# Performance work log

Measured on AMD Instinct MI355X. Metric: run time of the kernel, lower is better.

The kernel has to match this reference:

```python
import jax, jax.numpy as jnp
import numpy as np

DIM = 768
NUM_HEADS = 12


def setup_inputs() -> dict:
    key = jax.random.key(0)
    k1, k2, k3 = jax.random.split(key, 3)
    x = jax.random.normal(k1, (8, 32, 32, DIM), dtype=jnp.float32)
    # xavier_uniform-style init for kernels
    lim_qkv = float(np.sqrt(6.0 / (DIM + 3 * DIM)))
    lim_o = float(np.sqrt(6.0 / (DIM + DIM)))
    w_qkv = jax.random.uniform(k2, (DIM, 3 * DIM), jnp.float32, -lim_qkv, lim_qkv)
    w_o = jax.random.uniform(k3, (DIM, DIM), jnp.float32, -lim_o, lim_o)
    return {"x": x, "w_qkv": w_qkv, "w_o": w_o}


def reference(x, w_qkv, w_o):
    bs, h, w, c = x.shape
    n = h * w
    nh = NUM_HEADS
    hd = c // nh
    xt = x.reshape(bs, n, c)
    qkv = xt @ w_qkv                                   # [bs, n, 3c]
    qkv = qkv.reshape(bs, n, 3, nh, hd)
    qkv = jnp.transpose(qkv, (2, 0, 3, 1, 4))          # [3, bs, nh, n, hd]
    q, k, v = qkv[0], qkv[1], qkv[2]
    scale = hd ** -0.5
    attn = jnp.einsum('bhqd,bhkd->bhqk', q, k) * scale  # [bs, nh, n, n]
    attn = jax.nn.softmax(attn, axis=-1)
    out = jnp.einsum('bhqk,bhkd->bhqd', attn, v)       # [bs, nh, n, hd]
    out = out.swapaxes(1, 2).reshape(bs, n, c)
    out = out @ w_o
    side = int(n ** 0.5)
    return out.reshape(bs, side, side, -1)
```

## Files before the change

kernel.cpp:

```cpp
#include <hip/hip_runtime.h>
#include <hip/hip_bf16.h>
#include <stdint.h>
#include <math.h>

#define SEQ   1024
#define NHEAD 12
#define HD    64
#define CDIM  768
#define MTOK  8192
#define NQKV  2304
#define NPAIR 96

#define QSCALE 0.18033688011112042f

typedef uint16_t u16;
typedef __attribute__((ext_vector_type(8)))  __bf16 bf16x8;
typedef __attribute__((ext_vector_type(4)))  float  f32x4;
typedef __attribute__((ext_vector_type(16))) float  f32x16;

__device__ __forceinline__ u16 f32_to_bf16(float f) {
  union { float f; uint32_t u; } cv; cv.f = f;
  uint32_t u = cv.u;
  return (u16)((u + 0x7FFFu + ((u >> 16) & 1u)) >> 16);
}

__device__ __forceinline__ uint32_t cvt_pk_bf16(float lo, float hi) {
  uint32_t r;
  asm("v_cvt_pk_bf16_f32 %0, %1, %2" : "=v"(r) : "v"(lo), "v"(hi));
  return r;
}

__device__ __forceinline__ void pl32_swap(uint32_t& a, uint32_t& b) {
  asm("v_permlane32_swap_b32 %0, %1" : "+v"(a), "+v"(b));
}

__device__ __forceinline__ float vexp2(float x) {
  float r; asm("v_exp_f32 %0, %1" : "=v"(r) : "v"(x)); return r;
}
__device__ __forceinline__ float vmax3(float a, float b, float c) {
  float d; asm("v_max3_f32 %0, %1, %2, %3" : "=v"(d) : "v"(a), "v"(b), "v"(c)); return d;
}
__device__ __forceinline__ float vrcp(float x) {
  float r; asm("v_rcp_f32 %0, %1" : "=v"(r) : "v"(x)); return r;
}

__device__ __forceinline__ void load_lds16(const u16* g, u16* l) {
  __builtin_amdgcn_global_load_lds(
      (const __attribute__((address_space(1))) uint32_t*)g,
      (__attribute__((address_space(3))) uint32_t*)l, 16, 0, 0);
}

__device__ __forceinline__ bf16x8 ldsw(const u16* base, int r, int cb) {
  int byte = (r << 7) + cb;
  byte ^= ((r & 7) << 4);
  return *(const bf16x8*)((const char*)base + byte);
}

template<int NB>
__device__ __forceinline__ void stage_swz(const u16* __restrict__ g, u16* l, int tid) {
  #pragma unroll
  for (int i = 0; i < NB / 4096; ++i) {
    int F = i * 4096 + tid * 16;
    int S = F ^ (((F >> 7) & 7) << 4);
    load_lds16(g + (S >> 1), l + (F >> 1));
  }
}

__device__ __forceinline__ void stage_vt(const u16* __restrict__ vtb, u16* l, int kc, int tid) {
  #pragma unroll
  for (int i = 0; i < 2; ++i) {
    int F = i * 4096 + tid * 16;
    int S = F ^ (((F >> 7) & 7) << 4);
    int r = S >> 7;
    int cb = S & 127;
    load_lds16(vtb + ((size_t)r << 10) + (kc << 6) + (cb >> 1), l + (F >> 1));
  }
}

#define CVT_BLOCKS 3072
#define TQKV_BLOCKS 432
__global__ __launch_bounds__(256) void prep_kernel(const float* __restrict__ x,
                                                   u16* __restrict__ xb,
                                                   const float* __restrict__ wqkv,
                                                   u16* __restrict__ wqkvT,
                                                   const float* __restrict__ wo,
                                                   u16* __restrict__ woT) {
  __shared__ u16 t[64][66];
  int bid = blockIdx.x;
  int tid = threadIdx.x;

  if (bid < CVT_BLOCKS) {
    int i = bid * 256 + tid;
    const float4* p = (const float4*)x + (size_t)i * 2;
    float4 a = p[0], b = p[1];
    uint4 o;
    o.x = cvt_pk_bf16(a.x, a.y);
    o.y = cvt_pk_bf16(a.z, a.w);
    o.z = cvt_pk_bf16(b.x, b.y);
    o.w = cvt_pk_bf16(b.z, b.w);
    ((uint4*)xb)[i] = o;
    return;
  }

  const float* in;
  u16* outp;
  int N, bid2;
  if (bid < CVT_BLOCKS + TQKV_BLOCKS) {
    bid2 = bid - CVT_BLOCKS; in = wqkv; outp = wqkvT; N = NQKV;
  } else {
    bid2 = bid - CVT_BLOCKS - TQKV_BLOCKS; in = wo; outp = woT; N = CDIM;
  }
  const int K = CDIM, nbk = CDIM >> 6;
  int bk = bid2 % nbk, bn = bid2 / nbk;
  int k0 = bk << 6, n0 = bn << 6;
  #pragma unroll
  for (int i = 0; i < 16; ++i) {
    int idx = i * 256 + tid;
    int kr = idx >> 6, nc = idx & 63;
    t[kr][nc] = f32_to_bf16(in[(size_t)(k0 + kr) * N + n0 + nc]);
  }
  __syncthreads();
  #pragma unroll
  for (int i = 0; i < 16; ++i) {
    int idx = i * 256 + tid;
    int nr = idx >> 6, kc = idx & 63;
    outp[(size_t)(n0 + nr) * K + k0 + kc] = t[kc][nr];
  }
}

template<int EPI>
__global__ __launch_bounds__(256) void gemm_bt(const u16* __restrict__ A,
                                               const u16* __restrict__ Bt,
                                               float* __restrict__ Cf,
                                               u16* __restrict__ qb,
                                               u16* __restrict__ kb,
                                               u16* __restrict__ vb,
                                               int M, int N, int K) {
  __shared__ u16 SH[4][8192];

  int bid = blockIdx.x;
  int xcd = bid & 7, ii = bid >> 3;
  int tn = ii >> 3;
  int tm = (xcd << 3) + (ii & 7);
  int mBase = tm << 7, nBase = tn << 7;
  int tid = threadIdx.x;
  int lane = tid & 63, wid = tid >> 6;
  int wr = (wid >> 1) << 6, wc = (wid & 1) << 6;
  int lr = lane & 15, lk = lane >> 4;

  const int nk = K >> 6;

  auto STAGE = [&](int kt, int b) {
    #pragma unroll
    for (int i2 = 0; i2 < 4; ++i2) {
      int F = i2 * 4096 + tid * 16;
      int row = F >> 7;
      int cb  = (F & 127) ^ ((row & 7) << 4);
      load_lds16(A + (size_t)(mBase + row) * K + kt * 64 + (cb >> 1), &SH[b][F >> 1]);
    }
    #pragma unroll
    for (int i2 = 0; i2 < 4; ++i2) {
      int F = i2 * 4096 + tid * 16;
      int row = F >> 7;
      int cb  = (F & 127) ^ ((row & 7) << 4);
      load_lds16(Bt + (size_t)(nBase + row) * K + kt * 64 + (cb >> 1), &SH[2 + b][F >> 1]);
    }
  };

  f32x4 acc[4][4] = {};

  STAGE(0, 0);
  for (int kt = 0; kt < nk; ++kt) {
    const int cur = kt & 1;
    if (kt + 1 < nk) {
      STAGE(kt + 1, cur ^ 1);
      asm volatile("s_waitcnt vmcnt(8)" ::: "memory");
    } else {
      asm volatile("s_waitcnt vmcnt(0)" ::: "memory");
    }
    __builtin_amdgcn_s_barrier();
    asm volatile("" ::: "memory");

    #pragma unroll
    for (int kk = 0; kk < 2; ++kk) {
      bf16x8 af[4], bfr[4];
      #pragma unroll
      for (int i2 = 0; i2 < 4; ++i2)
        af[i2]  = ldsw(SH[cur], wr + i2 * 16 + lr, kk * 64 + lk * 16);
      #pragma unroll
      for (int i2 = 0; i2 < 4; ++i2)
        bfr[i2] = ldsw(SH[2 + cur], wc + i2 * 16 + lr, kk * 64 + lk * 16);
      #pragma unroll
      for (int mi = 0; mi < 4; ++mi)
        #pragma unroll
        for (int ni = 0; ni < 4; ++ni)
          acc[mi][ni] = __builtin_amdgcn_mfma_f32_16x16x32_bf16(af[mi], bfr[ni], acc[mi][ni], 0, 0, 0);
    }

    __builtin_amdgcn_s_barrier();
    asm volatile("" ::: "memory");
  }

  if (EPI == 0) {
    int c0 = nBase + wc;
    int s  = c0 / CDIM;
    int rem0 = c0 - s * CDIM, hh = rem0 >> 6;
    u16* ereg = &SH[0][0] + wid * 4096;

    #pragma unroll
    for (int mi = 0; mi < 4; ++mi)
      #pragma unroll
      for (int ni = 0; ni < 4; ++ni)
        #pragma unroll
        for (int j = 0; j < 4; ++j) {
          float val = acc[mi][ni][j];
          if (s == 0) val *= QSCALE;
          int mloc = mi * 16 + lk * 4 + j;
          int cloc = ni * 16 + lr;
          int rrow = (s == 2) ? cloc : mloc;
          int ccol = (s == 2) ? mloc : cloc;
          int byte = (rrow << 7) + (((ccol << 1)) ^ ((rrow & 7) << 4));
          *(u16*)((char*)ereg + byte) = f32_to_bf16(val);
        }

    u16* dst;
    if (s == 2) {
      int m0 = mBase + wr;
      int bb = m0 >> 10, nn0 = m0 & 1023;
      dst = vb + (((size_t)(bb * NHEAD + hh)) << 16) + ((size_t)lane << 10) + nn0;
    } else {
      int mrow = mBase + wr + lane;
      int bb = mrow >> 10, nn = mrow & 1023;
      u16* buf = (s == 0) ? qb : kb;
      dst = buf + (((size_t)(bb * NHEAD + hh)) << 16) + nn * 64;
    }
    #pragma unroll
    for (int ic = 0; ic < 8; ++ic) {
      int rc = (ic + (lane >> 3)) & 7;
      int byte = (lane << 7) + ((rc << 4) ^ ((lane & 7) << 4));
      bf16x8 vv = *(const bf16x8*)((const char*)ereg + byte);
      *(bf16x8*)(dst + rc * 8) = vv;
    }
  } else {
    char* ereg = (char*)(&SH[0][0]) + wid * 16384;
    #pragma unroll
    for (int mi = 0; mi < 4; ++mi)
      #pragma unroll
      for (int ni = 0; ni < 4; ++ni)
        #pragma unroll
        for (int j = 0; j < 4; ++j) {
          int rrow = mi * 16 + lk * 4 + j;
          int byte = (rrow << 8) + (((ni * 16 + lr) << 2) ^ ((rrow & 7) << 4));
          *(float*)(ereg + byte) = acc[mi][ni][j];
        }
    int mrow = mBase + wr + lane;
    float* dst = Cf + (size_t)mrow * N + (nBase + wc);
    #pragma unroll
    for (int ic = 0; ic < 16; ++ic) {
      int rc = (ic + ((lane >> 3) << 1)) & 15;
      int byte = (lane << 8) + ((rc << 4) ^ ((lane & 7) << 4));
      f32x4 vv = *(const f32x4*)(ereg + byte);
      *(f32x4*)(dst + rc * 4) = vv;
    }
  }
}

__global__ __launch_bounds__(256, 3) void attn_kernel(const u16* __restrict__ q,
                                                      const u16* __restrict__ k,
                                                      const u16* __restrict__ v,
                                                      u16* __restrict__ out) {
  __shared__ u16 Ks[2][4096];
  __shared__ u16 Vs[3][4096];

  int bid = blockIdx.x;
  int wgid = (bid & 7) * 96 + (bid >> 3);
  int pair = wgid >> 3;
  int qt   = wgid & 7;
  int b = pair / NHEAD, hh = pair - b * NHEAD;
  const u16* Kg  = k + ((size_t)pair << 16);
  const u16* Vtb = v + ((size_t)pair << 16);
  int tid = threadIdx.x, lane = tid & 63, wid = tid >> 6;
  int ql = lane & 31, hi = lane >> 5;

  const u16* Qrow = q + ((size_t)pair << 16) + (size_t)((qt << 7) + (wid << 5) + ql) * 64;
  bf16x8 qf[4];
  #pragma unroll
  for (int t = 0; t < 4; ++t)
    qf[t] = *(const bf16x8*)(Qrow + t * 16 + hi * 8);

  float m_ = -1e30f, l_ = 0.f;
  f32x16 acc0 = {}, acc1 = {};
  f32x16 pA0, pA1, pB0, pB1;

  auto SMPV = [&](f32x16& s0, f32x16& s1, const u16* vbase) {
    float a0 = vmax3(s0[0],  s0[1],  s0[2]);
    float a1 = vmax3(s0[3],  s0[4],  s0[5]);
    float a2 = vmax3(s0[6],  s0[7],  s0[8]);
    float a3 = vmax3(s0[9],  s0[10], s0[11]);
    float a4 = vmax3(s0[12], s0[13], s0[14]);
    float a5 = vmax3(s0[15], s1[0],  s1[1]);
    float a6 = vmax3(s1[2],  s1[3],  s1[4]);
    float a7 = vmax3(s1[5],  s1[6],  s1[7]);
    float a8 = vmax3(s1[8],  s1[9],  s1[10]);
    float a9 = vmax3(s1[11], s1[12], s1[13]);
    float aA = fmaxf(s1[14], s1[15]);
    float b0 = vmax3(a0, a1, a2);
    float b1 = vmax3(a3, a4, a5);
    float b2 = vmax3(a6, a7, a8);
    float b3 = vmax3(a9, aA, b0);
    float pm = vmax3(b1, b2, b3);

    if (!__all(pm - m_ <= 8.f)) {
      float om = fmaxf(pm, __shfl_xor(pm, 32, 64));
      float newm = fmaxf(m_, om);
      float alpha = vexp2(m_ - newm);
      m_ = newm;
      l_ *= alpha;
      #pragma unroll
      for (int r = 0; r < 16; ++r) {
        int qr = (r & 3) + 8 * (r >> 2) + 4 * hi;
        float ar = __shfl(alpha, qr, 32);
        acc0[r] *= ar;
        acc1[r] *= ar;
      }
    }

    #pragma unroll
    for (int r = 0; r < 16; ++r) s0[r] = vexp2(s0[r] - m_);
    #pragma unroll
    for (int r = 0; r < 16; ++r) s1[r] = vexp2(s1[r] - m_);

    {
      f32x16 ss = s0 + s1;
      float c0 = (ss[0] + ss[1]) + (ss[2] + ss[3]);
      float c1 = (ss[4] + ss[5]) + (ss[6] + ss[7]);
      float c2 = (ss[8] + ss[9]) + (ss[10] + ss[11]);
      float c3 = (ss[12] + ss[13]) + (ss[14] + ss[15]);
      l_ += (c0 + c1) + (c2 + c3);
    }

    __builtin_amdgcn_s_setprio(1);
    #pragma unroll
    for (int t = 0; t < 4; ++t) {
      const int base = (t & 1) * 8;
      uint32_t wA, wB, wC, wD;
      if (t < 2) {
        wA = cvt_pk_bf16(s0[base + 0], s0[base + 1]);
        wB = cvt_pk_bf16(s0[base + 2], s0[base + 3]);
        wC = cvt_pk_bf16(s0[base + 4], s0[base + 5]);
        wD = cvt_pk_bf16(s0[base + 6], s0[base + 7]);
      } else {
        wA = cvt_pk_bf16(s1[base + 0], s1[base + 1]);
        wB = cvt_pk_bf16(s1[base + 2], s1[base + 3]);
        wC = cvt_pk_bf16(s1[base + 4], s1[base + 5]);
        wD = cvt_pk_bf16(s1[base + 6], s1[base + 7]);
      }
      pl32_swap(wA, wC);
      pl32_swap(wB, wD);
      union { uint32_t u[4]; bf16x8 v8; } pu;
      pu.u[0] = wA; pu.u[1] = wB; pu.u[2] = wC; pu.u[3] = wD;
      bf16x8 v0 = ldsw(vbase, ql,      t * 32 + hi * 16);
      acc0 = __builtin_amdgcn_mfma_f32_32x32x16_bf16(pu.v8, v0, acc0, 0, 0, 0);
      bf16x8 v1 = ldsw(vbase, 32 + ql, t * 32 + hi * 16);
      acc1 = __builtin_amdgcn_mfma_f32_32x32x16_bf16(pu.v8, v1, acc1, 0, 0, 0);
    }
    __builtin_amdgcn_s_setprio(0);
  };

  auto QK = [&](int kc, f32x16& s0, f32x16& s1) {
    const u16* kbase = Ks[kc & 1];
    s0 = (f32x16){}; s1 = (f32x16){};
    __builtin_amdgcn_s_setprio(1);
    #pragma unroll
    for (int t = 0; t < 4; ++t) {
      bf16x8 k0 = ldsw(kbase, ql,      t * 32 + hi * 16);
      s0 = __builtin_amdgcn_mfma_f32_32x32x16_bf16(k0, qf[t], s0, 0, 0, 0);
      bf16x8 k1 = ldsw(kbase, 32 + ql, t * 32 + hi * 16);
      s1 = __builtin_amdgcn_mfma_f32_32x32x16_bf16(k1, qf[t], s1, 0, 0, 0);
    }
    __builtin_amdgcn_s_setprio(0);
  };

  auto TOP = [&](int kc) {
    if (kc < 15) {
      int nx = kc + 1;
      stage_swz<8192>(Kg + (nx << 12), Ks[nx & 1], tid);
      stage_vt(Vtb, Vs[nx % 3], nx, tid);
      asm volatile("s_waitcnt vmcnt(4)" ::: "memory");
    } else {
      asm volatile("s_waitcnt vmcnt(0)" ::: "memory");
    }
    __builtin_amdgcn_s_barrier();
    asm volatile("" ::: "memory");
  };
  auto BOT = [&]() {
    __builtin_amdgcn_s_barrier();
    asm volatile("" ::: "memory");
  };

  stage_swz<8192>(Kg, Ks[0], tid);
  stage_vt(Vtb, Vs[0], 0, tid);

  for (int kc2 = 0; kc2 < 16; kc2 += 2) {
    TOP(kc2);
    QK(kc2, pA0, pA1);
    if (kc2 > 0) SMPV(pB0, pB1, Vs[(kc2 + 2) % 3]);
    BOT();
    TOP(kc2 + 1);
    QK(kc2 + 1, pB0, pB1);
    SMPV(pA0, pA1, Vs[kc2 % 3]);
    BOT();
  }
  SMPV(pB0, pB1, Vs[0]);

  l_ += __shfl_xor(l_, 32, 64);
  float il = vrcp(l_);
  u16* ob = out + ((size_t)(b * SEQ + (qt << 7) + (wid << 5))) * CDIM + hh * 64 + ql;
  #pragma unroll
  for (int r = 0; r < 16; ++r) {
    int qr = (r & 3) + 8 * (r >> 2) + 4 * hi;
    float ilr = __shfl(il, qr, 32);
    ob[(size_t)qr * CDIM]      = f32_to_bf16(acc0[r] * ilr);
    ob[(size_t)qr * CDIM + 32] = f32_to_bf16(acc1[r] * ilr);
  }
}

extern "C" void kernel_launch(void* const* d_in, const int* in_sizes, int n_in,
                              void* d_out, int out_size, void* d_ws, size_t ws_size,
                              hipStream_t stream) {
  const float* x     = (const float*)d_in[0];
  const float* w_qkv = (const float*)d_in[1];
  const float* w_o   = (const float*)d_in[2];
  float* out = (float*)d_out;

  u16* xb    = (u16*)d_ws;
  u16* wqkvT = xb    + (size_t)MTOK * CDIM;
  u16* woT   = wqkvT + (size_t)NQKV * CDIM;
  u16* qb    = woT   + (size_t)CDIM * CDIM;
  u16* kb    = qb    + (size_t)NPAIR * SEQ * HD;
  u16* vb    = kb    + (size_t)NPAIR * SEQ * HD;
  u16* ao    = vb    + (size_t)NPAIR * SEQ * HD;

  prep_kernel<<<dim3(CVT_BLOCKS + TQKV_BLOCKS + 144), 256, 0, stream>>>(
      x, xb, w_qkv, wqkvT, w_o, woT);

  gemm_bt<0><<<dim3((MTOK / 128) * (NQKV / 128)), 256, 0, stream>>>(
      xb, wqkvT, nullptr, qb, kb, vb, MTOK, NQKV, CDIM);

  attn_kernel<<<dim3(NPAIR * 8), 256, 0, stream>>>(qb, kb, vb, ao);

  gemm_bt<1><<<dim3((MTOK / 128) * (CDIM / 128)), 256, 0, stream>>>(
      ao, woT, out, nullptr, nullptr, nullptr, MTOK, CDIM, CDIM);
}
```

Baseline: 121.2 us.

## Triple-buffer K tiles and merge barriers to one sync per step

The attention kernel's K shared-memory buffer grows from two to three slots, and the per-step TOP/BOT barrier pair becomes a single wait-and-barrier followed by issuing the next tile's loads. The goal is to halve the number of workgroup barriers and let the global loads for the next K/V tile overlap the current QK and PV MFMA work. In exchange, each step now waits for all outstanding loads (vmcnt(0)) before the barrier, which can expose load latency. The larger LDS footprint may also cut occupancy under the 3-blocks-per-CU launch bound.

```diff
diff --git a/kernel.cpp b/kernel.cpp
--- a/kernel.cpp
+++ b/kernel.cpp
@@ -269,7 +269,7 @@
                                                       const u16* __restrict__ k,
                                                       const u16* __restrict__ v,
                                                       u16* __restrict__ out) {
-  __shared__ u16 Ks[2][4096];
+  __shared__ u16 Ks[3][4096];
   __shared__ u16 Vs[3][4096];
 
   int bid = blockIdx.x;
@@ -367,8 +367,7 @@
     __builtin_amdgcn_s_setprio(0);
   };
 
-  auto QK = [&](int kc, f32x16& s0, f32x16& s1) {
-    const u16* kbase = Ks[kc & 1];
+  auto QK = [&](const u16* kbase, f32x16& s0, f32x16& s1) {
     s0 = (f32x16){}; s1 = (f32x16){};
     __builtin_amdgcn_s_setprio(1);
     #pragma unroll
@@ -381,35 +380,28 @@
     __builtin_amdgcn_s_setprio(0);
   };
 
-  auto TOP = [&](int kc) {
-    if (kc < 15) {
-      int nx = kc + 1;
-      stage_swz<8192>(Kg + (nx << 12), Ks[nx & 1], tid);
-      stage_vt(Vtb, Vs[nx % 3], nx, tid);
-      asm volatile("s_waitcnt vmcnt(4)" ::: "memory");
-    } else {
-      asm volatile("s_waitcnt vmcnt(0)" ::: "memory");
-    }
+  auto SYNC = [&]() {
+    asm volatile("s_waitcnt vmcnt(0)" ::: "memory");
     __builtin_amdgcn_s_barrier();
     asm volatile("" ::: "memory");
   };
-  auto BOT = [&]() {
-    __builtin_amdgcn_s_barrier();
-    asm volatile("" ::: "memory");
+  auto STAGE = [&](int kc) {
+    int sl = kc % 3;
+    stage_swz<8192>(Kg + (kc << 12), Ks[sl], tid);
+    stage_vt(Vtb, Vs[sl], kc, tid);
   };
 
-  stage_swz<8192>(Kg, Ks[0], tid);
-  stage_vt(Vtb, Vs[0], 0, tid);
+  STAGE(0);
 
   for (int kc2 = 0; kc2 < 16; kc2 += 2) {
-    TOP(kc2);
-    QK(kc2, pA0, pA1);
+    SYNC();
+    if (kc2 + 1 < 16) STAGE(kc2 + 1);
+    QK(Ks[kc2 % 3], pA0, pA1);
     if (kc2 > 0) SMPV(pB0, pB1, Vs[(kc2 + 2) % 3]);
-    BOT();
-    TOP(kc2 + 1);
-    QK(kc2 + 1, pB0, pB1);
+    SYNC();
+    if (kc2 + 2 < 16) STAGE(kc2 + 2);
+    QK(Ks[(kc2 + 1) % 3], pB0, pB1);
     SMPV(pA0, pA1, Vs[kc2 % 3]);
-    BOT();
   }
   SMPV(pB0, pB1, Vs[0]);
 
```

Result: no change. 121.5 us (+0.3%).
